# Performance work log

Measured on AMD Instinct MI355X. Metric: run time of the kernel, lower is better.

Reference implementation:

```python
import jax, jax.numpy as jnp
import numpy as np

N_HEAD, F_IN, F_OUT = 4, 768, 64
BS, N = 4, 2048


def setup_inputs() -> dict:
    key = jax.random.key(0)
    k_h, k_w, k_src, k_dst = jax.random.split(key, 4)
    # xavier_uniform bounds
    lim_w = float(np.sqrt(6.0 / (F_IN + F_OUT)))
    lim_a = float(np.sqrt(6.0 / (F_OUT + 1)))
    return {
        "h": jax.random.normal(k_h, (BS, N, F_IN), dtype=jnp.float32),
        "w": jax.random.uniform(k_w, (N_HEAD, F_IN, F_OUT), jnp.float32, -lim_w, lim_w),
        "a_src": jax.random.uniform(k_src, (N_HEAD, F_OUT, 1), jnp.float32, -lim_a, lim_a),
        "a_dst": jax.random.uniform(k_dst, (N_HEAD, F_OUT, 1), jnp.float32, -lim_a, lim_a),
        "bias": jnp.zeros((F_OUT,), dtype=jnp.float32),
    }


def reference(h, w, a_src, a_dst, bias):
    # h: [b, n, f_in]; w: [h, f_in, f_out]
    h_prime = jnp.einsum("bnf,hfo->bhno", h, w)          # [b, h, n, f_out]
    t = jnp.tanh(h_prime)
    attn_src = jnp.einsum("bhno,ho->bhn", t, a_src[..., 0])  # [b, h, n]
    attn_dst = jnp.einsum("bhno,ho->bhn", t, a_dst[..., 0])  # [b, h, n]
    # broadcast add: attn[b,h,i,j] = src[b,h,i] + dst[b,h,j]
    attn = attn_src[..., :, None] + attn_dst[..., None, :]   # [b, h, n, n]
    attn = jnp.where(attn >= 0, attn, 0.2 * attn)            # leaky_relu(0.2)
    attn = jax.nn.softmax(attn, axis=-1)
    out = jnp.einsum("bhij,bhjo->bhio", attn, h_prime)       # [b, h, n, f_out]
    return out + bias
```

## Files before the change

kernel.cpp:

```cpp
#include <hip/hip_runtime.h>
#include <hip/hip_bf16.h>

#define NHEAD 4
#define FIN   768
#define FOUT  64
#define BSZ   4
#define NSEQ  2048
#define BH    (BSZ*NHEAD)
#define LOG2E 1.44269504088896f

typedef __attribute__((ext_vector_type(8)))  short bf16x8;
typedef __attribute__((ext_vector_type(16))) float f32x16;
typedef __attribute__((ext_vector_type(8)))  unsigned short u16x8;
typedef __attribute__((ext_vector_type(4)))  unsigned short u16x4;
typedef __attribute__((ext_vector_type(4)))  unsigned u32x4;

__device__ __forceinline__ unsigned short f2bf(float f){
  unsigned b = __float_as_uint(f);
  return (unsigned short)((b + 0x7fffu + ((b >> 16) & 1u)) >> 16);
}
__device__ __forceinline__ unsigned fenc(float f){
  unsigned b = __float_as_uint(f);
  return (b & 0x80000000u) ? ~b : (b | 0x80000000u);
}
__device__ __forceinline__ float fdec(unsigned u){
  unsigned b = (u & 0x80000000u) ? (u ^ 0x80000000u) : ~u;
  return __uint_as_float(b);
}
__device__ __forceinline__ float fexp2(float x){
#if __has_builtin(__builtin_amdgcn_exp2f)
  return __builtin_amdgcn_exp2f(x);
#else
  return exp2f(x);
#endif
}
__device__ __forceinline__ unsigned pkbf(float lo, float hi){
#if __has_builtin(__builtin_amdgcn_cvt_pk_bf16_f32)
  typedef __attribute__((ext_vector_type(2))) __bf16 bf2;
  union { bf2 v; unsigned u; } cv;
  cv.v = __builtin_amdgcn_cvt_pk_bf16_f32(lo, hi);
  return cv.u;
#else
  return (unsigned)f2bf(lo) | ((unsigned)f2bf(hi) << 16);
#endif
}

__global__ __launch_bounds__(512) void k_prep_w(
    const float* __restrict__ w, unsigned short* __restrict__ wp,
    unsigned* __restrict__ dmaxe)
{
  if (blockIdx.x == 0 && threadIdx.x < BH) dmaxe[threadIdx.x] = 0;
  const int head = blockIdx.x & 3, kt = blockIdx.x >> 2;
  const int o = threadIdx.x & 63, c = threadIdx.x >> 6;
  const float* wsrc = w + (size_t)head*FIN*FOUT + (size_t)(kt*64 + c*8)*FOUT + o;
  u16x8 pk;
  #pragma unroll
  for (int j = 0; j < 8; ++j) pk[j] = f2bf(wsrc[(size_t)j*FOUT]);
  *(u16x8*)((char*)wp + ((size_t)((head*12 + kt)*64 + o))*128 + ((c ^ (o & 7)) << 4)) = pk;
}

__global__ __launch_bounds__(512, 2) void k_hprime(
    const float* __restrict__ h, const unsigned short* __restrict__ wp,
    const float* __restrict__ a_src, const float* __restrict__ a_dst,
    unsigned short* __restrict__ hpz2, float* __restrict__ srcv,
    float* __restrict__ dstv, unsigned* __restrict__ dmaxe)
{
  __shared__ __align__(16) char smem[65536];
  float* psumS = (float*)(smem + 16384);
  float* psumD = (float*)(smem + 16896);
  char*  Tt    = smem + 32768;

  const int tid  = threadIdx.x;
  const int bid  = blockIdx.x;
  const int bh1  = (bid & 7) | (((bid >> 3) & 1) << 3);
  const int head = bh1 & 3;
  const int jbase = (bid >> 4) << 6;
  const int i0a   = (bh1 >> 2)*NSEQ + jbase;
  const int wave = tid >> 6, lane = tid & 63;
  const int wm = wave & 1, wn = (wave >> 1) & 1, kw = wave >> 2;
  const int l32 = lane & 31, h32 = lane >> 5;

  f32x16 acc = {0,0,0,0,0,0,0,0,0,0,0,0,0,0,0,0};

  const int sr = tid >> 3, sc = tid & 7;
  const float* hA = h + (size_t)(i0a + sr)*FIN + sc*8;
  const char*  wB = (const char*)wp + ((size_t)(head*12*64 + sr))*128 + sc*16;
  const int aslot = (sc ^ (sr & 7)) << 4;

  float4 ra0 = *(const float4*)(hA);
  float4 ra1 = *(const float4*)(hA + 4);
  float4 ra2 = *(const float4*)(hA + 64);
  float4 ra3 = *(const float4*)(hA + 68);
  u16x8  rb0 = *(const u16x8*)(wB);
  u16x8  rb1 = *(const u16x8*)(wB + 8192);

  for (int it = 0; it < 6; ++it){
    char* Ab = smem + (it & 1)*16384;
    char* Bb = smem + 32768 + (it & 1)*16384;
    u32x4 pk0, pk1;
    pk0[0] = pkbf(ra0.x, ra0.y); pk0[1] = pkbf(ra0.z, ra0.w);
    pk0[2] = pkbf(ra1.x, ra1.y); pk0[3] = pkbf(ra1.z, ra1.w);
    pk1[0] = pkbf(ra2.x, ra2.y); pk1[1] = pkbf(ra2.z, ra2.w);
    pk1[2] = pkbf(ra3.x, ra3.y); pk1[3] = pkbf(ra3.z, ra3.w);
    *(u32x4*)(Ab + sr*256 + aslot)        = pk0;
    *(u32x4*)(Ab + sr*256 + 128 + aslot)  = pk1;
    *(u16x8*)(Bb + sr*256 + sc*16)        = rb0;
    *(u16x8*)(Bb + sr*256 + 128 + sc*16)  = rb1;
    __syncthreads();
    if (it < 5){
      const float* an = hA + (it+1)*128;
      ra0 = *(const float4*)(an);      ra1 = *(const float4*)(an + 4);
      ra2 = *(const float4*)(an + 64); ra3 = *(const float4*)(an + 68);
      const char* bn = wB + (size_t)(2*(it+1))*8192;
      rb0 = *(const u16x8*)(bn);       rb1 = *(const u16x8*)(bn + 8192);
    }
    #pragma unroll
    for (int s = 0; s < 4; ++s){
      const int slot = (((s*2 + h32) ^ (l32 & 7)) << 4);
      bf16x8 av = *(const bf16x8*)(Ab + (wm*32 + l32)*256 + kw*128 + slot);
      bf16x8 bv = *(const bf16x8*)(Bb + (wn*32 + l32)*256 + kw*128 + slot);
      acc = __builtin_amdgcn_mfma_f32_32x32x16_bf16(av, bv, acc, 0, 0, 0);
    }
    __syncthreads();
  }

  if (kw == 1) *(f32x16*)(smem + (size_t)((wave & 3)*64 + lane)*64) = acc;
  __syncthreads();
  if (kw == 0){
    acc += *(const f32x16*)(smem + (size_t)((wave & 3)*64 + lane)*64);
    const float as = a_src[head*64 + wn*32 + l32];
    const float ad = a_dst[head*64 + wn*32 + l32];
    #pragma unroll
    for (int rb = 0; rb < 4; ++rb){
      const int jb = wm*32 + rb*8 + h32*4;
      u16x4 c4;
      #pragma unroll
      for (int q = 0; q < 4; ++q){
        const float v = acc[rb*4 + q];
        c4[q] = f2bf(v);
        const float t = tanhf(v);
        float ps = t*as, pd = t*ad;
        ps += __shfl_xor(ps, 1);  ps += __shfl_xor(ps, 2);  ps += __shfl_xor(ps, 4);
        ps += __shfl_xor(ps, 8);  ps += __shfl_xor(ps, 16);
        pd += __shfl_xor(pd, 1);  pd += __shfl_xor(pd, 2);  pd += __shfl_xor(pd, 4);
        pd += __shfl_xor(pd, 8);  pd += __shfl_xor(pd, 16);
        if (l32 == 0){
          psumS[(jb + q)*2 + wn] = ps;
          psumD[(jb + q)*2 + wn] = pd;
        }
      }
      const int orow = wn*32 + l32;
      const int slot = ((jb >> 3) & 7) ^ (orow & 7);
      *(u16x4*)(Tt + orow*128 + slot*16 + (jb & 7)*2) = c4;
    }
  }
  __syncthreads();

  {
    const int o = tid & 63, c = tid >> 6;
    u16x8 val = *(const u16x8*)(Tt + o*128 + ((c ^ (o & 7)) << 4));
    *(u16x8*)((char*)hpz2 + ((size_t)(bh1*256 + (jbase >> 3) + c)*64 + o)*16) = val;
  }
  if (tid < 64){
    float sv = (psumS[tid*2] + psumS[tid*2 + 1]) * LOG2E;
    float dv = (psumD[tid*2] + psumD[tid*2 + 1]) * LOG2E;
    srcv[(size_t)bh1*NSEQ + jbase + tid] = sv;
    dstv[(size_t)bh1*NSEQ + jbase + tid] = dv;
    float dmx = dv;
    dmx = fmaxf(dmx, __shfl_xor(dmx, 1));  dmx = fmaxf(dmx, __shfl_xor(dmx, 2));
    dmx = fmaxf(dmx, __shfl_xor(dmx, 4));  dmx = fmaxf(dmx, __shfl_xor(dmx, 8));
    dmx = fmaxf(dmx, __shfl_xor(dmx, 16)); dmx = fmaxf(dmx, __shfl_xor(dmx, 32));
    if (tid == 0) atomicMax(&dmaxe[bh1], fenc(dmx));
  }
}

__global__ __launch_bounds__(512, 4) void k_attn(
    const unsigned short* __restrict__ hpz2, const float* __restrict__ srcv,
    const float* __restrict__ dstv, const unsigned* __restrict__ dmaxe,
    const float* __restrict__ bias, float* __restrict__ out)
{
  __shared__ __align__(16) char smem[33792];
  float* Lbuf = (float*)(smem + 32768);

  const int tid = threadIdx.x;
  const int bid = blockIdx.x;
  const int bh  = (bid & 7) | (((bid >> 3) & 1) << 3);
  const int i0  = (bid >> 4) << 6;
  const int wave = tid >> 6, lane = tid & 63;
  const int wm = wave & 1, jw = wave >> 1;
  const int l32 = lane & 31, h32 = lane >> 5;

  const float s2  = srcv[(size_t)bh*NSEQ + i0 + wm*32 + l32];
  const float dm2 = fdec(dmaxe[bh]);
  float m2 = s2 + dm2; m2 = fmaxf(m2, 0.2f*m2);
  const float u_ = s2 - m2;
  const float v_ = 0.2f*s2 - m2;
  const float* dptr = dstv + (size_t)bh*NSEQ;

  const u16x8* gp = (const u16x8*)((const char*)hpz2 + (size_t)bh*256*64*16);

  f32x16 accO0 = {0,0,0,0,0,0,0,0,0,0,0,0,0,0,0,0};
  f32x16 accO1 = {0,0,0,0,0,0,0,0,0,0,0,0,0,0,0,0};
  float lpart = 0.f;

  *(u16x8*)(smem + tid*16)         = gp[tid];
  *(u16x8*)(smem + (tid + 512)*16) = gp[tid + 512];
  __syncthreads();

  for (int w = 0; w < 16; ++w){
    char* cur = smem + (w & 1)*16384;
    char* nxt = smem + ((w + 1) & 1)*16384;
    u16x8 r0, r1;
    if (w < 15){
      r0 = gp[(w+1)*1024 + tid];
      r1 = gp[(w+1)*1024 + tid + 512];
    }
    #pragma unroll
    for (int stl = 0; stl < 2; ++stl){
      const int Jl = jw*4 + stl*2 + h32;
      const int j0 = (w*16 + Jl)*8;
      float4 d0 = *(const float4*)(dptr + j0);
      float4 d1 = *(const float4*)(dptr + j0 + 4);
      float e0,e1,e2,e3,e4,e5,e6,e7;
      e0 = fexp2(fmaxf(u_ + d0.x, fmaf(0.2f, d0.x, v_)));
      e1 = fexp2(fmaxf(u_ + d0.y, fmaf(0.2f, d0.y, v_)));
      e2 = fexp2(fmaxf(u_ + d0.z, fmaf(0.2f, d0.z, v_)));
      e3 = fexp2(fmaxf(u_ + d0.w, fmaf(0.2f, d0.w, v_)));
      e4 = fexp2(fmaxf(u_ + d1.x, fmaf(0.2f, d1.x, v_)));
      e5 = fexp2(fmaxf(u_ + d1.y, fmaf(0.2f, d1.y, v_)));
      e6 = fexp2(fmaxf(u_ + d1.z, fmaf(0.2f, d1.z, v_)));
      e7 = fexp2(fmaxf(u_ + d1.w, fmaf(0.2f, d1.w, v_)));
      lpart += ((e0+e1)+(e2+e3)) + ((e4+e5)+(e6+e7));
      u32x4 pk;
      pk[0] = pkbf(e0, e1); pk[1] = pkbf(e2, e3);
      pk[2] = pkbf(e4, e5); pk[3] = pkbf(e6, e7);
      const bf16x8 pA = __builtin_bit_cast(bf16x8, pk);
      const bf16x8 bv0 = *(const bf16x8*)(cur + (Jl*64 +      l32)*16);
      const bf16x8 bv1 = *(const bf16x8*)(cur + (Jl*64 + 32 + l32)*16);
      accO0 = __builtin_amdgcn_mfma_f32_32x32x16_bf16(pA, bv0, accO0, 0, 0, 0);
      accO1 = __builtin_amdgcn_mfma_f32_32x32x16_bf16(pA, bv1, accO1, 0, 0, 0);
    }
    if (w < 15){
      *(u16x8*)(nxt + tid*16)         = r0;
      *(u16x8*)(nxt + (tid + 512)*16) = r1;
    }
    __syncthreads();
  }

  lpart += __shfl_xor(lpart, 32);
  if (lane < 32) Lbuf[(wm*4 + jw)*32 + l32] = lpart;

  const float4 bia = *(const float4*)(bias + (tid & 15)*4);
  #pragma unroll
  for (int ph = 0; ph < 2; ++ph){
    __syncthreads();
    if (wm == ph){
      float* ob = (float*)smem;
      #pragma unroll
      for (int reg = 0; reg < 16; ++reg){
        const int m = (reg & 3) + 8*(reg >> 2) + 4*h32;
        ob[(jw*32 + m)*64 +      l32] = accO0[reg];
        ob[(jw*32 + m)*64 + 32 + l32] = accO1[reg];
      }
    }
    __syncthreads();
    {
      const int i = tid >> 4, o4 = (tid & 15)*4;
      const float* ob = (const float*)smem;
      float4 v0 = *(const float4*)(ob + (0*32 + i)*64 + o4);
      float4 v1 = *(const float4*)(ob + (1*32 + i)*64 + o4);
      float4 v2 = *(const float4*)(ob + (2*32 + i)*64 + o4);
      float4 v3 = *(const float4*)(ob + (3*32 + i)*64 + o4);
      const float l = Lbuf[(ph*4+0)*32 + i] + Lbuf[(ph*4+1)*32 + i]
                    + Lbuf[(ph*4+2)*32 + i] + Lbuf[(ph*4+3)*32 + i];
      const float r = 1.f / l;
      float4 res;
      res.x = (v0.x + v1.x + v2.x + v3.x)*r + bia.x;
      res.y = (v0.y + v1.y + v2.y + v3.y)*r + bia.y;
      res.z = (v0.z + v1.z + v2.z + v3.z)*r + bia.z;
      res.w = (v0.w + v1.w + v2.w + v3.w)*r + bia.w;
      *(float4*)(out + ((size_t)bh*NSEQ + i0 + ph*32 + i)*64 + o4) = res;
    }
  }
}

extern "C" void kernel_launch(void* const* d_in, const int* in_sizes, int n_in,
                              void* d_out, int out_size, void* d_ws, size_t ws_size,
                              hipStream_t stream)
{
  const float* h     = (const float*)d_in[0];
  const float* w     = (const float*)d_in[1];
  const float* a_src = (const float*)d_in[2];
  const float* a_dst = (const float*)d_in[3];
  const float* bias  = (const float*)d_in[4];
  float* out = (float*)d_out;

  char* ws = (char*)d_ws;
  unsigned short* hpz2 = (unsigned short*)ws;
  float* srcv = (float*)(ws + (4u<<20));
  float* dstv = (float*)(ws + (4u<<20) + (128u<<10));
  unsigned short* wp = (unsigned short*)(ws + (4u<<20) + (256u<<10));
  unsigned* dmaxe = (unsigned*)(ws + (4u<<20) + (640u<<10));

  k_prep_w<<<48, 512, 0, stream>>>(w, wp, dmaxe);
  k_hprime<<<512, 512, 0, stream>>>(h, wp, a_src, a_dst, hpz2, srcv, dstv, dmaxe);
  k_attn<<<512, 512, 0, stream>>>(hpz2, srcv, dstv, dmaxe, bias, out);
}
```

Measured before the change: 125.9 us.

## Fuse weight conversion into hprime kernel and drop softmax max pass

Removes the separate weight-prep kernel; each hprime block now reads fp32 W directly and converts it to bf16 while staging it into shared memory. It also drops the global per-head max of the dst scores (atomicMax plus decode) and the max-subtraction in the softmax, relying on tanh keeping scores bounded so exp2 cannot overflow. The redundant trailing barrier in the double-buffered K loop is removed as well. The aim is to save a kernel launch, atomics and a sync per iteration. The cost is more redundant W loads and conversions per block, and numerical safety now depends on the magnitude of a_src and a_dst.

```diff
diff --git a/kernel.cpp b/kernel.cpp
--- a/kernel.cpp
+++ b/kernel.cpp
@@ -18,14 +18,6 @@
 __device__ __forceinline__ unsigned short f2bf(float f){
   unsigned b = __float_as_uint(f);
   return (unsigned short)((b + 0x7fffu + ((b >> 16) & 1u)) >> 16);
-}
-__device__ __forceinline__ unsigned fenc(float f){
-  unsigned b = __float_as_uint(f);
-  return (b & 0x80000000u) ? ~b : (b | 0x80000000u);
-}
-__device__ __forceinline__ float fdec(unsigned u){
-  unsigned b = (u & 0x80000000u) ? (u ^ 0x80000000u) : ~u;
-  return __uint_as_float(b);
 }
 __device__ __forceinline__ float fexp2(float x){
 #if __has_builtin(__builtin_amdgcn_exp2f)
@@ -45,25 +37,11 @@
 #endif
 }
 
-__global__ __launch_bounds__(512) void k_prep_w(
-    const float* __restrict__ w, unsigned short* __restrict__ wp,
-    unsigned* __restrict__ dmaxe)
-{
-  if (blockIdx.x == 0 && threadIdx.x < BH) dmaxe[threadIdx.x] = 0;
-  const int head = blockIdx.x & 3, kt = blockIdx.x >> 2;
-  const int o = threadIdx.x & 63, c = threadIdx.x >> 6;
-  const float* wsrc = w + (size_t)head*FIN*FOUT + (size_t)(kt*64 + c*8)*FOUT + o;
-  u16x8 pk;
-  #pragma unroll
-  for (int j = 0; j < 8; ++j) pk[j] = f2bf(wsrc[(size_t)j*FOUT]);
-  *(u16x8*)((char*)wp + ((size_t)((head*12 + kt)*64 + o))*128 + ((c ^ (o & 7)) << 4)) = pk;
-}
-
 __global__ __launch_bounds__(512, 2) void k_hprime(
-    const float* __restrict__ h, const unsigned short* __restrict__ wp,
+    const float* __restrict__ h, const float* __restrict__ w,
     const float* __restrict__ a_src, const float* __restrict__ a_dst,
     unsigned short* __restrict__ hpz2, float* __restrict__ srcv,
-    float* __restrict__ dstv, unsigned* __restrict__ dmaxe)
+    float* __restrict__ dstv)
 {
   __shared__ __align__(16) char smem[65536];
   float* psumS = (float*)(smem + 16384);
@@ -84,18 +62,25 @@
 
   const int sr = tid >> 3, sc = tid & 7;
   const float* hA = h + (size_t)(i0a + sr)*FIN + sc*8;
-  const char*  wB = (const char*)wp + ((size_t)(head*12*64 + sr))*128 + sc*16;
   const int aslot = (sc ^ (sr & 7)) << 4;
+
+  const int ob = tid & 63, cc = tid >> 6;
+  const float* wsrc = w + (size_t)head*FIN*FOUT + ob;
+  const int bslot0 = ((cc & 7) ^ (ob & 7)) << 4;
 
   float4 ra0 = *(const float4*)(hA);
   float4 ra1 = *(const float4*)(hA + 4);
   float4 ra2 = *(const float4*)(hA + 64);
   float4 ra3 = *(const float4*)(hA + 68);
-  u16x8  rb0 = *(const u16x8*)(wB);
-  u16x8  rb1 = *(const u16x8*)(wB + 8192);
+  float rb[16];
+  #pragma unroll
+  for (int j = 0; j < 8; ++j){
+    rb[j]     = wsrc[(size_t)(cc*8 + j)*FOUT];
+    rb[8 + j] = wsrc[(size_t)(64 + cc*8 + j)*FOUT];
+  }
 
   for (int it = 0; it < 6; ++it){
-    char* Ab = smem + (it & 1)*16384;
+    char* Ab = smem +         (it & 1)*16384;
     char* Bb = smem + 32768 + (it & 1)*16384;
     u32x4 pk0, pk1;
     pk0[0] = pkbf(ra0.x, ra0.y); pk0[1] = pkbf(ra0.z, ra0.w);
@@ -104,15 +89,24 @@
     pk1[2] = pkbf(ra3.x, ra3.y); pk1[3] = pkbf(ra3.z, ra3.w);
     *(u32x4*)(Ab + sr*256 + aslot)        = pk0;
     *(u32x4*)(Ab + sr*256 + 128 + aslot)  = pk1;
-    *(u16x8*)(Bb + sr*256 + sc*16)        = rb0;
-    *(u16x8*)(Bb + sr*256 + 128 + sc*16)  = rb1;
+    u32x4 qb0, qb1;
+    qb0[0] = pkbf(rb[0],  rb[1]);  qb0[1] = pkbf(rb[2],  rb[3]);
+    qb0[2] = pkbf(rb[4],  rb[5]);  qb0[3] = pkbf(rb[6],  rb[7]);
+    qb1[0] = pkbf(rb[8],  rb[9]);  qb1[1] = pkbf(rb[10], rb[11]);
+    qb1[2] = pkbf(rb[12], rb[13]); qb1[3] = pkbf(rb[14], rb[15]);
+    *(u32x4*)(Bb + ob*256 +       bslot0) = qb0;
+    *(u32x4*)(Bb + ob*256 + 128 + bslot0) = qb1;
     __syncthreads();
     if (it < 5){
       const float* an = hA + (it+1)*128;
       ra0 = *(const float4*)(an);      ra1 = *(const float4*)(an + 4);
       ra2 = *(const float4*)(an + 64); ra3 = *(const float4*)(an + 68);
-      const char* bn = wB + (size_t)(2*(it+1))*8192;
-      rb0 = *(const u16x8*)(bn);       rb1 = *(const u16x8*)(bn + 8192);
+      const float* wn_ = wsrc + (size_t)(it+1)*128*FOUT;
+      #pragma unroll
+      for (int j = 0; j < 8; ++j){
+        rb[j]     = wn_[(size_t)(cc*8 + j)*FOUT];
+        rb[8 + j] = wn_[(size_t)(64 + cc*8 + j)*FOUT];
+      }
     }
     #pragma unroll
     for (int s = 0; s < 4; ++s){
@@ -121,7 +115,6 @@
       bf16x8 bv = *(const bf16x8*)(Bb + (wn*32 + l32)*256 + kw*128 + slot);
       acc = __builtin_amdgcn_mfma_f32_32x32x16_bf16(av, bv, acc, 0, 0, 0);
     }
-    __syncthreads();
   }
 
   if (kw == 1) *(f32x16*)(smem + (size_t)((wave & 3)*64 + lane)*64) = acc;
@@ -131,12 +124,12 @@
     const float as = a_src[head*64 + wn*32 + l32];
     const float ad = a_dst[head*64 + wn*32 + l32];
     #pragma unroll
-    for (int rb = 0; rb < 4; ++rb){
-      const int jb = wm*32 + rb*8 + h32*4;
+    for (int rb2 = 0; rb2 < 4; ++rb2){
+      const int jb = wm*32 + rb2*8 + h32*4;
       u16x4 c4;
       #pragma unroll
       for (int q = 0; q < 4; ++q){
-        const float v = acc[rb*4 + q];
+        const float v = acc[rb2*4 + q];
         c4[q] = f2bf(v);
         const float t = tanhf(v);
         float ps = t*as, pd = t*ad;
@@ -162,22 +155,15 @@
     *(u16x8*)((char*)hpz2 + ((size_t)(bh1*256 + (jbase >> 3) + c)*64 + o)*16) = val;
   }
   if (tid < 64){
-    float sv = (psumS[tid*2] + psumS[tid*2 + 1]) * LOG2E;
-    float dv = (psumD[tid*2] + psumD[tid*2 + 1]) * LOG2E;
-    srcv[(size_t)bh1*NSEQ + jbase + tid] = sv;
-    dstv[(size_t)bh1*NSEQ + jbase + tid] = dv;
-    float dmx = dv;
-    dmx = fmaxf(dmx, __shfl_xor(dmx, 1));  dmx = fmaxf(dmx, __shfl_xor(dmx, 2));
-    dmx = fmaxf(dmx, __shfl_xor(dmx, 4));  dmx = fmaxf(dmx, __shfl_xor(dmx, 8));
-    dmx = fmaxf(dmx, __shfl_xor(dmx, 16)); dmx = fmaxf(dmx, __shfl_xor(dmx, 32));
-    if (tid == 0) atomicMax(&dmaxe[bh1], fenc(dmx));
+    srcv[(size_t)bh1*NSEQ + jbase + tid] = (psumS[tid*2] + psumS[tid*2 + 1]) * LOG2E;
+    dstv[(size_t)bh1*NSEQ + jbase + tid] = (psumD[tid*2] + psumD[tid*2 + 1]) * LOG2E;
   }
 }
 
 __global__ __launch_bounds__(512, 4) void k_attn(
     const unsigned short* __restrict__ hpz2, const float* __restrict__ srcv,
-    const float* __restrict__ dstv, const unsigned* __restrict__ dmaxe,
-    const float* __restrict__ bias, float* __restrict__ out)
+    const float* __restrict__ dstv, const float* __restrict__ bias,
+    float* __restrict__ out)
 {
   __shared__ __align__(16) char smem[33792];
   float* Lbuf = (float*)(smem + 32768);
@@ -190,11 +176,9 @@
   const int wm = wave & 1, jw = wave >> 1;
   const int l32 = lane & 31, h32 = lane >> 5;
 
-  const float s2  = srcv[(size_t)bh*NSEQ + i0 + wm*32 + l32];
-  const float dm2 = fdec(dmaxe[bh]);
-  float m2 = s2 + dm2; m2 = fmaxf(m2, 0.2f*m2);
-  const float u_ = s2 - m2;
-  const float v_ = 0.2f*s2 - m2;
+  const float s2 = srcv[(size_t)bh*NSEQ + i0 + wm*32 + l32];
+  const float u_ = s2;
+  const float v_ = 0.2f*s2;
   const float* dptr = dstv + (size_t)bh*NSEQ;
 
   const u16x8* gp = (const u16x8*)((const char*)hpz2 + (size_t)bh*256*64*16);
@@ -299,10 +283,7 @@
   unsigned short* hpz2 = (unsigned short*)ws;
   float* srcv = (float*)(ws + (4u<<20));
   float* dstv = (float*)(ws + (4u<<20) + (128u<<10));
-  unsigned short* wp = (unsigned short*)(ws + (4u<<20) + (256u<<10));
-  unsigned* dmaxe = (unsigned*)(ws + (4u<<20) + (640u<<10));
-
-  k_prep_w<<<48, 512, 0, stream>>>(w, wp, dmaxe);
-  k_hprime<<<512, 512, 0, stream>>>(h, wp, a_src, a_dst, hpz2, srcv, dstv, dmaxe);
-  k_attn<<<512, 512, 0, stream>>>(hpz2, srcv, dstv, dmaxe, bias, out);
-}
+
+  k_hprime<<<512, 512, 0, stream>>>(h, w, a_src, a_dst, hpz2, srcv, dstv);
+  k_attn<<<512, 512, 0, stream>>>(hpz2, srcv, dstv, bias, out);
+}
```

After: 119.3 us. -5.2%, faster.
